# Kernel tuning notes

Hardware: AMD Instinct MI355X
Metric: run time of the kernel (lower is better)

Reference implementation:

```python
import jax, jax.numpy as jnp
import numpy as np

E, T, H, I = 64, 2048, 512, 1024


def setup_inputs() -> dict:
    key = jax.random.key(0)
    k1, k2, k3 = jax.random.split(key, 3)
    x = jax.random.normal(k1, (T, E, H), dtype=jnp.float32)
    # trunc_normal_(std=sqrt(0.1/fan_in)) approximated by normal with same std
    wi = jax.random.normal(k2, (E, H, I), dtype=jnp.float32) * (0.1 / H) ** 0.5
    wo = jax.random.normal(k3, (E, I, H), dtype=jnp.float32) * (0.1 / I) ** 0.5
    return {"x": x, "wi": wi, "wo": wo}


def reference(x, wi, wo):
    # x: [T, E, H] -> transpose to [E, T, H] (reshape(e,-1,h) is a no-op for 3D input)
    xt = jnp.transpose(x, (1, 0, 2))
    # expert GEMM 1 + exact GELU (torch nn.GELU default is erf-based)
    h = jax.nn.gelu(jnp.einsum('eth,ehi->eti', xt, wi), approximate=False)
    # dropout is skipped when expert_parallel is None; grad scalers are identity (ep_size=1)
    out = jnp.einsum('eti,eih->eth', h, wo)
    return jnp.transpose(out, (1, 0, 2))  # back to [T, E, H]
```

## Files before the change

### kernel.cpp

```cpp
#include <hip/hip_runtime.h>
#include <stdint.h>

#define NE 64
#define NT 2048
#define NH 512
#define NI 1024

typedef __attribute__((ext_vector_type(8))) short bf16x8;
typedef __attribute__((ext_vector_type(4))) float f32x4;

typedef const __attribute__((address_space(1))) void* gptr1_t;
typedef __attribute__((address_space(3))) void* lptr3_t;
#define GLOAD16(g, l) \
  __builtin_amdgcn_global_load_lds((gptr1_t)(const void*)(g), (lptr3_t)(void*)(l), 16, 0, 0)

static __device__ __forceinline__ uint16_t f2bf(float f) {
  uint32_t u = __builtin_bit_cast(uint32_t, f);
  u += 0x7fffu + ((u >> 16) & 1u);
  return (uint16_t)(u >> 16);
}

static __device__ __forceinline__ float gelu_erf(float v) {
  return 0.5f * v * (1.0f + erff(v * 0.7071067811865475f));
}

__global__ __launch_bounds__(256)
void cast_x(const float* __restrict__ x, uint16_t* __restrict__ xB,
            int t_start, int S) {
  const int total = S * NE * (NH / 8);
  for (int c = blockIdx.x * 256 + threadIdx.x; c < total; c += gridDim.x * 256) {
    const int hb = c & 63;
    const int e = (c >> 6) & 63;
    const int t = c >> 12;
    const float* ip = x + ((size_t)(t_start + t) * NE + e) * NH + (hb << 3);
    const f32x4 v0 = *(const f32x4*)ip;
    const f32x4 v1 = *(const f32x4*)(ip + 4);
    bf16x8 w;
#pragma unroll
    for (int u = 0; u < 4; ++u) {
      w[u] = (short)f2bf(v0[u]);
      w[u + 4] = (short)f2bf(v1[u]);
    }
    *(bf16x8*)&xB[((size_t)e * S + t) * NH + (hb << 3)] = w;
  }
}

__global__ __launch_bounds__(256)
void conv_tr(const float* __restrict__ in, uint16_t* __restrict__ out, int K, int N) {
  const int e = blockIdx.x;
  const int k0 = blockIdx.y << 6;
  const int n0 = blockIdx.z << 6;
  __shared__ uint16_t t[64][72];
  const int tid = threadIdx.x;
  const int r = tid >> 2;
  const int c0 = (tid & 3) << 4;
  const float* ip = in + ((size_t)e * K + k0 + r) * N + n0 + c0;
#pragma unroll
  for (int j = 0; j < 16; j += 4) {
    f32x4 v = *(const f32x4*)(ip + j);
#pragma unroll
    for (int u = 0; u < 4; ++u) t[c0 + j + u][r] = f2bf(v[u]);
  }
  __syncthreads();
  uint16_t* op = out + ((size_t)e * N + n0 + r) * K + k0 + c0;
  *(bf16x8*)op = *(const bf16x8*)&t[r][c0];
  *(bf16x8*)(op + 8) = *(const bf16x8*)&t[r][c0 + 8];
}

__global__ __launch_bounds__(256, 3)
void k_gemm1(const uint16_t* __restrict__ xB, const uint16_t* __restrict__ wiB,
             uint16_t* __restrict__ h, int Ts) {
  const int Mt = Ts >> 7;
  const int nwg = gridDim.x;
  const int wid = (blockIdx.x & 7) * (nwg >> 3) + (blockIdx.x >> 3);
  const int bn = wid & 7;
  const int bm = (wid >> 3) % Mt;
  const int be = wid / (Mt << 3);
  const int t0 = bm << 7, n0 = bn << 7;

  __shared__ __align__(16) uint16_t As[8192];
  __shared__ __align__(16) uint16_t Bs[8192];

  const int tid = threadIdx.x, lane = tid & 63;
  const int wy = (tid >> 7) & 1, wx = (tid >> 6) & 1;

  const uint16_t* Abase = xB + ((size_t)be * Ts + t0) * NH;
  const uint16_t* Bbase = wiB + ((size_t)be * NI + n0) * NH;

  int off[4], ldsOff[4];
#pragma unroll
  for (int s = 0; s < 4; ++s) {
    const int c = (s << 8) + tid;
    const int rr = c >> 3, kgs = c & 7;
    off[s] = (rr << 9) + ((kgs ^ (rr & 7)) << 3);
    ldsOff[s] = c << 4;
  }

  f32x4 acc[4][4];
#pragma unroll
  for (int i = 0; i < 4; ++i)
#pragma unroll
    for (int j = 0; j < 4; ++j) acc[i][j] = (f32x4){0.f, 0.f, 0.f, 0.f};

  const int KIT = NH >> 6;
  for (int it = 0; it < KIT; ++it) {
    __syncthreads();
#pragma unroll
    for (int s = 0; s < 4; ++s)
      GLOAD16(Abase + (it << 6) + off[s], (char*)As + ldsOff[s]);
#pragma unroll
    for (int s = 0; s < 4; ++s)
      GLOAD16(Bbase + (it << 6) + off[s], (char*)Bs + ldsOff[s]);
    __syncthreads();
#pragma unroll
    for (int ks = 0; ks < 2; ++ks) {
      const int kg = (ks << 2) + (lane >> 4);
      bf16x8 af[4], bfr[4];
#pragma unroll
      for (int mi = 0; mi < 4; ++mi) {
        const int row = (wy << 6) + (mi << 4) + (lane & 15);
        af[mi] = *(const bf16x8*)&As[(row << 6) + ((kg ^ (row & 7)) << 3)];
      }
#pragma unroll
      for (int ni = 0; ni < 4; ++ni) {
        const int col = (wx << 6) + (ni << 4) + (lane & 15);
        bfr[ni] = *(const bf16x8*)&Bs[(col << 6) + ((kg ^ (col & 7)) << 3)];
      }
#pragma unroll
      for (int mi = 0; mi < 4; ++mi)
#pragma unroll
        for (int ni = 0; ni < 4; ++ni)
          acc[mi][ni] = __builtin_amdgcn_mfma_f32_16x16x32_bf16(
              af[mi], bfr[ni], acc[mi][ni], 0, 0, 0);
    }
  }

#pragma unroll
  for (int mi = 0; mi < 4; ++mi) {
#pragma unroll
    for (int ni = 0; ni < 4; ++ni) {
      const int col = n0 + (wx << 6) + (ni << 4) + (lane & 15);
#pragma unroll
      for (int j = 0; j < 4; ++j) {
        const int r = t0 + (wy << 6) + (mi << 4) + ((lane >> 4) << 2) + j;
        h[((size_t)be * Ts + r) * NI + col] = f2bf(gelu_erf(acc[mi][ni][j]));
      }
    }
  }
}

__global__ __launch_bounds__(256, 3)
void k_gemm2(const uint16_t* __restrict__ hA, const uint16_t* __restrict__ woB,
             float* __restrict__ out, int t_start, int Ts) {
  const int Mt = Ts >> 7;
  const int nwg = gridDim.x;
  const int wid = (blockIdx.x & 7) * (nwg >> 3) + (blockIdx.x >> 3);
  const int bn = wid & 3;
  const int bm = (wid >> 2) % Mt;
  const int be = wid / (Mt << 2);
  const int t0 = bm << 7, n0 = bn << 7;

  __shared__ __align__(16) uint16_t As[8192];
  __shared__ __align__(16) uint16_t Bs[8192];

  const int tid = threadIdx.x, lane = tid & 63;
  const int wy = (tid >> 7) & 1, wx = (tid >> 6) & 1;

  const uint16_t* Abase = hA + ((size_t)be * Ts + t0) * NI;
  const uint16_t* Bbase = woB + ((size_t)be * NH + n0) * NI;

  int off[4], ldsOff[4];
#pragma unroll
  for (int s = 0; s < 4; ++s) {
    const int c = (s << 8) + tid;
    const int rr = c >> 3, kgs = c & 7;
    off[s] = (rr << 10) + ((kgs ^ (rr & 7)) << 3);
    ldsOff[s] = c << 4;
  }

  f32x4 acc[4][4];
#pragma unroll
  for (int i = 0; i < 4; ++i)
#pragma unroll
    for (int j = 0; j < 4; ++j) acc[i][j] = (f32x4){0.f, 0.f, 0.f, 0.f};

  const int KIT = NI >> 6;
  for (int it = 0; it < KIT; ++it) {
    __syncthreads();
#pragma unroll
    for (int s = 0; s < 4; ++s)
      GLOAD16(Abase + (it << 6) + off[s], (char*)As + ldsOff[s]);
#pragma unroll
    for (int s = 0; s < 4; ++s)
      GLOAD16(Bbase + (it << 6) + off[s], (char*)Bs + ldsOff[s]);
    __syncthreads();
#pragma unroll
    for (int ks = 0; ks < 2; ++ks) {
      const int kg = (ks << 2) + (lane >> 4);
      bf16x8 af[4], bfr[4];
#pragma unroll
      for (int mi = 0; mi < 4; ++mi) {
        const int row = (wy << 6) + (mi << 4) + (lane & 15);
        af[mi] = *(const bf16x8*)&As[(row << 6) + ((kg ^ (row & 7)) << 3)];
      }
#pragma unroll
      for (int ni = 0; ni < 4; ++ni) {
        const int col = (wx << 6) + (ni << 4) + (lane & 15);
        bfr[ni] = *(const bf16x8*)&Bs[(col << 6) + ((kg ^ (col & 7)) << 3)];
      }
#pragma unroll
      for (int mi = 0; mi < 4; ++mi)
#pragma unroll
        for (int ni = 0; ni < 4; ++ni)
          acc[mi][ni] = __builtin_amdgcn_mfma_f32_16x16x32_bf16(
              af[mi], bfr[ni], acc[mi][ni], 0, 0, 0);
    }
  }

#pragma unroll
  for (int mi = 0; mi < 4; ++mi) {
#pragma unroll
    for (int ni = 0; ni < 4; ++ni) {
      const int col = n0 + (wx << 6) + (ni << 4) + (lane & 15);
#pragma unroll
      for (int j = 0; j < 4; ++j) {
        const int r = t0 + (wy << 6) + (mi << 4) + ((lane >> 4) << 2) + j;
        out[((size_t)(t_start + r) * NE + be) * NH + col] = acc[mi][ni][j];
      }
    }
  }
}

extern "C" void kernel_launch(void* const* d_in, const int* in_sizes, int n_in,
                              void* d_out, int out_size, void* d_ws, size_t ws_size,
                              hipStream_t stream) {
  const float* x = (const float*)d_in[0];
  const float* wi = (const float*)d_in[1];
  const float* wo = (const float*)d_in[2];
  float* out = (float*)d_out;

  uint16_t* wiB = (uint16_t*)d_ws;
  uint16_t* woB = (uint16_t*)((char*)d_ws + 67108864);
  char* rest = (char*)d_ws + 134217728;

  const size_t perRow = (size_t)NE * NH * 2 + (size_t)NE * NI * 2;
  size_t avail = (ws_size > 134217728u) ? ws_size - 134217728u : 0;
  int Ts = (int)(avail / perRow);
  Ts &= ~127;
  if (Ts > NT) Ts = NT;
  if (Ts < 128) Ts = 128;

  uint16_t* xB = (uint16_t*)rest;
  uint16_t* h = (uint16_t*)(rest + (size_t)NE * Ts * NH * 2);

  hipLaunchKernelGGL(conv_tr, dim3(NE, NH / 64, NI / 64), dim3(256), 0, stream,
                     wi, wiB, NH, NI);
  hipLaunchKernelGGL(conv_tr, dim3(NE, NI / 64, NH / 64), dim3(256), 0, stream,
                     wo, woB, NI, NH);

  for (int ts = 0; ts < NT; ts += Ts) {
    int cur = NT - ts;
    if (cur > Ts) cur = Ts;
    const int Mt = cur >> 7;
    const int castGrid = (cur * NE * (NH / 8) + 255) / 256;
    hipLaunchKernelGGL(cast_x, dim3(castGrid < 2048 ? castGrid : 2048), dim3(256),
                       0, stream, x, xB, ts, cur);
    hipLaunchKernelGGL(k_gemm1, dim3(Mt * 8 * NE), dim3(256), 0, stream,
                       xB, wiB, h, cur);
    hipLaunchKernelGGL(k_gemm2, dim3(Mt * 4 * NE), dim3(256), 0, stream,
                       h, woB, out, ts, cur);
  }
}
```

Measured before the change: 563.9 us.

## Replace GEMM kernels with 256x256-tile double-buffered pipelined MFMA kernel

Replaces the two separate 128x128 single-buffered GEMM kernels with one templated kernel using 256x256 tiles, 512 threads (8 waves), and double-buffered LDS. Global-to-LDS loads for the next K-step are interleaved with MFMA phases using explicit waitcnt, barriers, sched_barrier, and setprio. The aim is to hide load latency and raise arithmetic intensity per workgroup. In exchange it uses 128KB of LDS and more registers, which lowers occupancy, and the tile count per expert is reduced.

Result: slower. 625.9 us (+11.0%).

```diff
diff --git a/kernel.cpp b/kernel.cpp
--- a/kernel.cpp
+++ b/kernel.cpp
@@ -67,165 +67,188 @@
   *(bf16x8*)(op + 8) = *(const bf16x8*)&t[r][c0 + 8];
 }
 
-__global__ __launch_bounds__(256, 3)
-void k_gemm1(const uint16_t* __restrict__ xB, const uint16_t* __restrict__ wiB,
-             uint16_t* __restrict__ h, int Ts) {
-  const int Mt = Ts >> 7;
+template <int KIT, int NTILES, int ASTR, int BSTR, bool GELU>
+__global__ __launch_bounds__(512, 2)
+void k_mm(const uint16_t* __restrict__ Ag, const uint16_t* __restrict__ Bg,
+          void* __restrict__ outp, int t_start, int Ts) {
+  const int Mt = Ts >> 8;
   const int nwg = gridDim.x;
-  const int wid = (blockIdx.x & 7) * (nwg >> 3) + (blockIdx.x >> 3);
-  const int bn = wid & 7;
-  const int bm = (wid >> 3) % Mt;
-  const int be = wid / (Mt << 3);
-  const int t0 = bm << 7, n0 = bn << 7;
-
-  __shared__ __align__(16) uint16_t As[8192];
-  __shared__ __align__(16) uint16_t Bs[8192];
-
-  const int tid = threadIdx.x, lane = tid & 63;
-  const int wy = (tid >> 7) & 1, wx = (tid >> 6) & 1;
-
-  const uint16_t* Abase = xB + ((size_t)be * Ts + t0) * NH;
-  const uint16_t* Bbase = wiB + ((size_t)be * NI + n0) * NH;
-
-  int off[4], ldsOff[4];
-#pragma unroll
-  for (int s = 0; s < 4; ++s) {
-    const int c = (s << 8) + tid;
-    const int rr = c >> 3, kgs = c & 7;
-    off[s] = (rr << 9) + ((kgs ^ (rr & 7)) << 3);
-    ldsOff[s] = c << 4;
-  }
-
-  f32x4 acc[4][4];
-#pragma unroll
-  for (int i = 0; i < 4; ++i)
+  const int wid_ = (blockIdx.x & 7) * (nwg >> 3) + (blockIdx.x >> 3);
+  const int bn = wid_ & (NTILES - 1);
+  const int bm = (wid_ / NTILES) % Mt;
+  const int be = wid_ / (NTILES * Mt);
+  const int t0 = bm << 8, n0 = bn << 8;
+
+  __shared__ __align__(16) uint16_t As[2][16384];
+  __shared__ __align__(16) uint16_t Bs[2][16384];
+
+  const int tid = threadIdx.x;
+  const int lane = tid & 63;
+  const int wv = tid >> 6;
+  const int wm = wv >> 2;
+  const int wn = wv & 3;
+  const int fr = lane & 15;
+  const int fq = lane >> 4;
+
+  const uint16_t* Abase = Ag + ((size_t)be * Ts + t0) * ASTR;
+  const uint16_t* Bbase = Bg + ((size_t)be * (NTILES * 256) + n0) * BSTR;
+
+  int aoff[2], boff[2];
+#pragma unroll
+  for (int s = 0; s < 2; ++s) {
+    const int c = tid + (s << 9);
+    const int row = c >> 3, g = c & 7;
+    aoff[s] = row * ASTR + ((g ^ (row & 7)) << 3);
+    boff[s] = row * BSTR + ((g ^ (row & 7)) << 3);
+  }
+
+  auto stageA = [&](int kt, int b, int h) {
+    const uint16_t* src = Abase + (size_t)(h << 7) * ASTR + (kt << 6);
+    char* dst = (char*)&As[b][0] + (h << 14) + (tid << 4);
+    GLOAD16(src + aoff[0], dst);
+    GLOAD16(src + aoff[1], dst + 8192);
+  };
+  auto stageB = [&](int kt, int b, int h) {
+    const uint16_t* src = Bbase + (size_t)(h << 7) * BSTR + (kt << 6);
+    char* dst = (char*)&Bs[b][0] + (h << 14) + (tid << 4);
+    GLOAD16(src + boff[0], dst);
+    GLOAD16(src + boff[1], dst + 8192);
+  };
+
+  auto ldsA = [&](int b, int mi, int ks) -> bf16x8 {
+    const int r = (mi << 4) + fr;
+    const int kg = ((ks << 2) + fq) ^ (fr & 7);
+    return *(const bf16x8*)&As[b][(wm << 13) + (r << 6) + (kg << 3)];
+  };
+  auto ldsB = [&](int b, int ni, int ks) -> bf16x8 {
+    const int r = ((wn & 1) << 6) + (ni << 4) + fr;
+    const int kg = ((ks << 2) + fq) ^ (fr & 7);
+    return *(const bf16x8*)&Bs[b][((wn >> 1) << 13) + (r << 6) + (kg << 3)];
+  };
+
+  f32x4 acc[8][4];
+#pragma unroll
+  for (int i = 0; i < 8; ++i)
 #pragma unroll
     for (int j = 0; j < 4; ++j) acc[i][j] = (f32x4){0.f, 0.f, 0.f, 0.f};
 
-  const int KIT = NH >> 6;
-  for (int it = 0; it < KIT; ++it) {
-    __syncthreads();
-#pragma unroll
-    for (int s = 0; s < 4; ++s)
-      GLOAD16(Abase + (it << 6) + off[s], (char*)As + ldsOff[s]);
-#pragma unroll
-    for (int s = 0; s < 4; ++s)
-      GLOAD16(Bbase + (it << 6) + off[s], (char*)Bs + ldsOff[s]);
-    __syncthreads();
-#pragma unroll
-    for (int ks = 0; ks < 2; ++ks) {
-      const int kg = (ks << 2) + (lane >> 4);
-      bf16x8 af[4], bfr[4];
-#pragma unroll
-      for (int mi = 0; mi < 4; ++mi) {
-        const int row = (wy << 6) + (mi << 4) + (lane & 15);
-        af[mi] = *(const bf16x8*)&As[(row << 6) + ((kg ^ (row & 7)) << 3)];
-      }
+  bf16x8 af[4][2], bfr[4][2];
+
+  stageA(0, 0, 0);
+  stageA(0, 0, 1);
+  stageB(0, 0, 0);
+  stageB(0, 0, 1);
+  stageB(1, 1, 0);
+  stageB(1, 1, 1);
+
+  for (int T = 0; T < KIT; ++T) {
+    const int rb = T & 1;
+    const int c1 = (T + 1 < KIT) ? T + 1 : KIT - 1;
+    const int c2 = (T + 2 < KIT) ? T + 2 : KIT - 1;
+
+    stageA(c1, (T + 1) & 1, 0);
+    asm volatile("s_waitcnt vmcnt(6)" ::: "memory");
+    __builtin_amdgcn_sched_barrier(0);
+    __builtin_amdgcn_s_barrier();
+    __builtin_amdgcn_sched_barrier(0);
+#pragma unroll
+    for (int mi = 0; mi < 4; ++mi)
+#pragma unroll
+      for (int ks = 0; ks < 2; ++ks) af[mi][ks] = ldsA(rb, mi, ks);
+#pragma unroll
+    for (int ni = 0; ni < 2; ++ni)
+#pragma unroll
+      for (int ks = 0; ks < 2; ++ks) bfr[ni][ks] = ldsB(rb, ni, ks);
+    __builtin_amdgcn_s_setprio(1);
+#pragma unroll
+    for (int mi = 0; mi < 4; ++mi)
+#pragma unroll
+      for (int ni = 0; ni < 2; ++ni)
+#pragma unroll
+        for (int ks = 0; ks < 2; ++ks)
+          acc[mi][ni] = __builtin_amdgcn_mfma_f32_16x16x32_bf16(
+              af[mi][ks], bfr[ni][ks], acc[mi][ni], 0, 0, 0);
+    __builtin_amdgcn_s_setprio(0);
+    __builtin_amdgcn_s_barrier();
+    __builtin_amdgcn_sched_barrier(0);
+
+    stageA(c1, (T + 1) & 1, 1);
+#pragma unroll
+    for (int ni = 2; ni < 4; ++ni)
+#pragma unroll
+      for (int ks = 0; ks < 2; ++ks) bfr[ni][ks] = ldsB(rb, ni, ks);
+    __builtin_amdgcn_s_setprio(1);
+#pragma unroll
+    for (int mi = 0; mi < 4; ++mi)
+#pragma unroll
+      for (int ni = 2; ni < 4; ++ni)
+#pragma unroll
+        for (int ks = 0; ks < 2; ++ks)
+          acc[mi][ni] = __builtin_amdgcn_mfma_f32_16x16x32_bf16(
+              af[mi][ks], bfr[ni][ks], acc[mi][ni], 0, 0, 0);
+    __builtin_amdgcn_s_setprio(0);
+    __builtin_amdgcn_s_barrier();
+    __builtin_amdgcn_sched_barrier(0);
+
+    stageB(c2, rb, 0);
+#pragma unroll
+    for (int mi = 0; mi < 4; ++mi)
+#pragma unroll
+      for (int ks = 0; ks < 2; ++ks) af[mi][ks] = ldsA(rb, mi + 4, ks);
+    __builtin_amdgcn_s_setprio(1);
+#pragma unroll
+    for (int mi = 0; mi < 4; ++mi)
+#pragma unroll
+      for (int ni = 0; ni < 2; ++ni)
+#pragma unroll
+        for (int ks = 0; ks < 2; ++ks)
+          acc[mi + 4][ni] = __builtin_amdgcn_mfma_f32_16x16x32_bf16(
+              af[mi][ks], bfr[ni][ks], acc[mi + 4][ni], 0, 0, 0);
+    __builtin_amdgcn_s_setprio(0);
+    __builtin_amdgcn_s_barrier();
+    __builtin_amdgcn_sched_barrier(0);
+
+    stageB(c2, rb, 1);
+    __builtin_amdgcn_s_setprio(1);
+#pragma unroll
+    for (int mi = 0; mi < 4; ++mi)
+#pragma unroll
+      for (int ni = 2; ni < 4; ++ni)
+#pragma unroll
+        for (int ks = 0; ks < 2; ++ks)
+          acc[mi + 4][ni] = __builtin_amdgcn_mfma_f32_16x16x32_bf16(
+              af[mi][ks], bfr[ni][ks], acc[mi + 4][ni], 0, 0, 0);
+    __builtin_amdgcn_s_setprio(0);
+    __builtin_amdgcn_s_barrier();
+    __builtin_amdgcn_sched_barrier(0);
+  }
+
+  if constexpr (GELU) {
+    uint16_t* hp = (uint16_t*)outp;
+#pragma unroll
+    for (int mi = 0; mi < 8; ++mi) {
 #pragma unroll
       for (int ni = 0; ni < 4; ++ni) {
-        const int col = (wx << 6) + (ni << 4) + (lane & 15);
-        bfr[ni] = *(const bf16x8*)&Bs[(col << 6) + ((kg ^ (col & 7)) << 3)];
-      }
-#pragma unroll
-      for (int mi = 0; mi < 4; ++mi)
-#pragma unroll
-        for (int ni = 0; ni < 4; ++ni)
-          acc[mi][ni] = __builtin_amdgcn_mfma_f32_16x16x32_bf16(
-              af[mi], bfr[ni], acc[mi][ni], 0, 0, 0);
-    }
-  }
-
-#pragma unroll
-  for (int mi = 0; mi < 4; ++mi) {
-#pragma unroll
-    for (int ni = 0; ni < 4; ++ni) {
-      const int col = n0 + (wx << 6) + (ni << 4) + (lane & 15);
-#pragma unroll
-      for (int j = 0; j < 4; ++j) {
-        const int r = t0 + (wy << 6) + (mi << 4) + ((lane >> 4) << 2) + j;
-        h[((size_t)be * Ts + r) * NI + col] = f2bf(gelu_erf(acc[mi][ni][j]));
+        const int col = n0 + (wn << 6) + (ni << 4) + fr;
+#pragma unroll
+        for (int j = 0; j < 4; ++j) {
+          const int row = t0 + (wm << 7) + (mi << 4) + (fq << 2) + j;
+          hp[((size_t)be * Ts + row) * NI + col] = f2bf(gelu_erf(acc[mi][ni][j]));
+        }
       }
     }
-  }
-}
-
-__global__ __launch_bounds__(256, 3)
-void k_gemm2(const uint16_t* __restrict__ hA, const uint16_t* __restrict__ woB,
-             float* __restrict__ out, int t_start, int Ts) {
-  const int Mt = Ts >> 7;
-  const int nwg = gridDim.x;
-  const int wid = (blockIdx.x & 7) * (nwg >> 3) + (blockIdx.x >> 3);
-  const int bn = wid & 3;
-  const int bm = (wid >> 2) % Mt;
-  const int be = wid / (Mt << 2);
-  const int t0 = bm << 7, n0 = bn << 7;
-
-  __shared__ __align__(16) uint16_t As[8192];
-  __shared__ __align__(16) uint16_t Bs[8192];
-
-  const int tid = threadIdx.x, lane = tid & 63;
-  const int wy = (tid >> 7) & 1, wx = (tid >> 6) & 1;
-
-  const uint16_t* Abase = hA + ((size_t)be * Ts + t0) * NI;
-  const uint16_t* Bbase = woB + ((size_t)be * NH + n0) * NI;
-
-  int off[4], ldsOff[4];
-#pragma unroll
-  for (int s = 0; s < 4; ++s) {
-    const int c = (s << 8) + tid;
-    const int rr = c >> 3, kgs = c & 7;
-    off[s] = (rr << 10) + ((kgs ^ (rr & 7)) << 3);
-    ldsOff[s] = c << 4;
-  }
-
-  f32x4 acc[4][4];
-#pragma unroll
-  for (int i = 0; i < 4; ++i)
-#pragma unroll
-    for (int j = 0; j < 4; ++j) acc[i][j] = (f32x4){0.f, 0.f, 0.f, 0.f};
-
-  const int KIT = NI >> 6;
-  for (int it = 0; it < KIT; ++it) {
-    __syncthreads();
-#pragma unroll
-    for (int s = 0; s < 4; ++s)
-      GLOAD16(Abase + (it << 6) + off[s], (char*)As + ldsOff[s]);
-#pragma unroll
-    for (int s = 0; s < 4; ++s)
-      GLOAD16(Bbase + (it << 6) + off[s], (char*)Bs + ldsOff[s]);
-    __syncthreads();
-#pragma unroll
-    for (int ks = 0; ks < 2; ++ks) {
-      const int kg = (ks << 2) + (lane >> 4);
-      bf16x8 af[4], bfr[4];
-#pragma unroll
-      for (int mi = 0; mi < 4; ++mi) {
-        const int row = (wy << 6) + (mi << 4) + (lane & 15);
-        af[mi] = *(const bf16x8*)&As[(row << 6) + ((kg ^ (row & 7)) << 3)];
-      }
+  } else {
+    float* op = (float*)outp;
+#pragma unroll
+    for (int mi = 0; mi < 8; ++mi) {
 #pragma unroll
       for (int ni = 0; ni < 4; ++ni) {
-        const int col = (wx << 6) + (ni << 4) + (lane & 15);
-        bfr[ni] = *(const bf16x8*)&Bs[(col << 6) + ((kg ^ (col & 7)) << 3)];
-      }
-#pragma unroll
-      for (int mi = 0; mi < 4; ++mi)
-#pragma unroll
-        for (int ni = 0; ni < 4; ++ni)
-          acc[mi][ni] = __builtin_amdgcn_mfma_f32_16x16x32_bf16(
-              af[mi], bfr[ni], acc[mi][ni], 0, 0, 0);
-    }
-  }
-
-#pragma unroll
-  for (int mi = 0; mi < 4; ++mi) {
-#pragma unroll
-    for (int ni = 0; ni < 4; ++ni) {
-      const int col = n0 + (wx << 6) + (ni << 4) + (lane & 15);
-#pragma unroll
-      for (int j = 0; j < 4; ++j) {
-        const int r = t0 + (wy << 6) + (mi << 4) + ((lane >> 4) << 2) + j;
-        out[((size_t)(t_start + r) * NE + be) * NH + col] = acc[mi][ni][j];
+        const int col = n0 + (wn << 6) + (ni << 4) + fr;
+#pragma unroll
+        for (int j = 0; j < 4; ++j) {
+          const int row = t0 + (wm << 7) + (mi << 4) + (fq << 2) + j;
+          op[((size_t)(t_start + row) * NE + be) * NH + col] = acc[mi][ni][j];
+        }
       }
     }
   }
@@ -246,12 +269,9 @@
   const size_t perRow = (size_t)NE * NH * 2 + (size_t)NE * NI * 2;
   size_t avail = (ws_size > 134217728u) ? ws_size - 134217728u : 0;
   int Ts = (int)(avail / perRow);
-  Ts &= ~127;
+  Ts &= ~255;
   if (Ts > NT) Ts = NT;
-  if (Ts < 128) Ts = 128;
-
-  uint16_t* xB = (uint16_t*)rest;
-  uint16_t* h = (uint16_t*)(rest + (size_t)NE * Ts * NH * 2);
+  if (Ts < 256) Ts = 256;
 
   hipLaunchKernelGGL(conv_tr, dim3(NE, NH / 64, NI / 64), dim3(256), 0, stream,
                      wi, wiB, NH, NI);
@@ -261,13 +281,15 @@
   for (int ts = 0; ts < NT; ts += Ts) {
     int cur = NT - ts;
     if (cur > Ts) cur = Ts;
-    const int Mt = cur >> 7;
+    const int Mt = cur >> 8;
+    uint16_t* xB = (uint16_t*)rest;
+    uint16_t* h = (uint16_t*)(rest + (size_t)NE * cur * NH * 2);
     const int castGrid = (cur * NE * (NH / 8) + 255) / 256;
     hipLaunchKernelGGL(cast_x, dim3(castGrid < 2048 ? castGrid : 2048), dim3(256),
                        0, stream, x, xB, ts, cur);
-    hipLaunchKernelGGL(k_gemm1, dim3(Mt * 8 * NE), dim3(256), 0, stream,
-                       xB, wiB, h, cur);
-    hipLaunchKernelGGL(k_gemm2, dim3(Mt * 4 * NE), dim3(256), 0, stream,
-                       h, woB, out, ts, cur);
-  }
-}
+    hipLaunchKernelGGL((k_mm<8, 4, NH, NH, true>), dim3(Mt * 4 * NE), dim3(512),
+                       0, stream, xB, wiB, (void*)h, 0, cur);
+    hipLaunchKernelGGL((k_mm<16, 2, NI, NI, false>), dim3(Mt * 2 * NE), dim3(512),
+                       0, stream, h, woB, (void*)out, ts, cur);
+  }
+}
```

## Load B fragments directly from global into registers with double-buffered prefetch

Applied to the files above, without the earlier changes.

Merges the two GEMM kernels into one template and stops staging the weight (B) tile through LDS. Each wave now reads its B fragments straight from global memory into registers, double-buffered so the next k-step's B loads overlap the current MFMA work. Only A still goes through LDS, which halves LDS use and LDS traffic. The cost is uncoalesced-ish 16-byte global reads of B with no reuse between the two wy waves, plus higher register pressure from two B buffers at a 3-waves occupancy target.

Result: slower. 793.1 us (+40.6%).

```diff
diff --git a/kernel.cpp b/kernel.cpp
--- a/kernel.cpp
+++ b/kernel.cpp
@@ -67,165 +67,114 @@
   *(bf16x8*)(op + 8) = *(const bf16x8*)&t[r][c0 + 8];
 }
 
+template <int KIT, int NTILES, int STR, bool GELU>
 __global__ __launch_bounds__(256, 3)
-void k_gemm1(const uint16_t* __restrict__ xB, const uint16_t* __restrict__ wiB,
-             uint16_t* __restrict__ h, int Ts) {
+void k_mm(const uint16_t* __restrict__ Ag, const uint16_t* __restrict__ Bg,
+          void* __restrict__ outp, int t_start, int Ts) {
   const int Mt = Ts >> 7;
   const int nwg = gridDim.x;
   const int wid = (blockIdx.x & 7) * (nwg >> 3) + (blockIdx.x >> 3);
-  const int bn = wid & 7;
-  const int bm = (wid >> 3) % Mt;
-  const int be = wid / (Mt << 3);
+  const int bn = wid & (NTILES - 1);
+  const int bm = (wid / NTILES) % Mt;
+  const int be = wid / (NTILES * Mt);
   const int t0 = bm << 7, n0 = bn << 7;
 
   __shared__ __align__(16) uint16_t As[8192];
-  __shared__ __align__(16) uint16_t Bs[8192];
 
   const int tid = threadIdx.x, lane = tid & 63;
   const int wy = (tid >> 7) & 1, wx = (tid >> 6) & 1;
-
-  const uint16_t* Abase = xB + ((size_t)be * Ts + t0) * NH;
-  const uint16_t* Bbase = wiB + ((size_t)be * NI + n0) * NH;
-
-  int off[4], ldsOff[4];
+  const int fr = lane & 15, fq = lane >> 4;
+
+  const uint16_t* Abase = Ag + ((size_t)be * Ts + t0) * STR;
+  const uint16_t* Bbase = Bg + ((size_t)be * (NTILES * 128) + n0) * STR;
+
+  int aoff[4], ldsOff[4];
 #pragma unroll
   for (int s = 0; s < 4; ++s) {
     const int c = (s << 8) + tid;
     const int rr = c >> 3, kgs = c & 7;
-    off[s] = (rr << 9) + ((kgs ^ (rr & 7)) << 3);
+    aoff[s] = rr * STR + ((kgs ^ (rr & 7)) << 3);
     ldsOff[s] = c << 4;
   }
 
+  const uint16_t* bp[4];
+#pragma unroll
+  for (int ni = 0; ni < 4; ++ni)
+    bp[ni] = Bbase + (size_t)((wx << 6) + (ni << 4) + fr) * STR + (fq << 3);
+
   f32x4 acc[4][4];
 #pragma unroll
   for (int i = 0; i < 4; ++i)
 #pragma unroll
     for (int j = 0; j < 4; ++j) acc[i][j] = (f32x4){0.f, 0.f, 0.f, 0.f};
 
-  const int KIT = NH >> 6;
-  for (int it = 0; it < KIT; ++it) {
-    __syncthreads();
+  bf16x8 b0[4][2], b1[4][2];
+
+  auto stageA = [&](int it) {
 #pragma unroll
     for (int s = 0; s < 4; ++s)
-      GLOAD16(Abase + (it << 6) + off[s], (char*)As + ldsOff[s]);
-#pragma unroll
-    for (int s = 0; s < 4; ++s)
-      GLOAD16(Bbase + (it << 6) + off[s], (char*)Bs + ldsOff[s]);
-    __syncthreads();
-#pragma unroll
-    for (int ks = 0; ks < 2; ++ks) {
-      const int kg = (ks << 2) + (lane >> 4);
-      bf16x8 af[4], bfr[4];
-#pragma unroll
-      for (int mi = 0; mi < 4; ++mi) {
-        const int row = (wy << 6) + (mi << 4) + (lane & 15);
-        af[mi] = *(const bf16x8*)&As[(row << 6) + ((kg ^ (row & 7)) << 3)];
-      }
+      GLOAD16(Abase + (it << 6) + aoff[s], (char*)As + ldsOff[s]);
+  };
+#define LOADB(buf, it)                                                        \
+  _Pragma("unroll") for (int ni = 0; ni < 4; ++ni)                            \
+      _Pragma("unroll") for (int ks = 0; ks < 2; ++ks)                        \
+          buf[ni][ks] = *(const bf16x8*)(bp[ni] + ((it) << 6) + (ks << 5));
+#define COMPUTE(buf)                                                          \
+  _Pragma("unroll") for (int ks = 0; ks < 2; ++ks) {                          \
+    const int kg = (ks << 2) + fq;                                            \
+    bf16x8 af[4];                                                             \
+    _Pragma("unroll") for (int mi = 0; mi < 4; ++mi) {                        \
+      const int row = (wy << 6) + (mi << 4) + fr;                             \
+      af[mi] = *(const bf16x8*)&As[(row << 6) + ((kg ^ (row & 7)) << 3)];     \
+    }                                                                         \
+    _Pragma("unroll") for (int mi = 0; mi < 4; ++mi)                          \
+        _Pragma("unroll") for (int ni = 0; ni < 4; ++ni)                      \
+            acc[mi][ni] = __builtin_amdgcn_mfma_f32_16x16x32_bf16(            \
+                af[mi], buf[ni][ks], acc[mi][ni], 0, 0, 0);                   \
+  }
+
+  LOADB(b0, 0);
+  for (int it = 0; it < KIT; it += 2) {
+    __syncthreads();
+    stageA(it);
+    __syncthreads();
+    LOADB(b1, it + 1);
+    COMPUTE(b0);
+    __syncthreads();
+    stageA(it + 1);
+    __syncthreads();
+    if (it + 2 < KIT) LOADB(b0, it + 2);
+    COMPUTE(b1);
+  }
+#undef LOADB
+#undef COMPUTE
+
+  if constexpr (GELU) {
+    uint16_t* hp = (uint16_t*)outp;
+#pragma unroll
+    for (int mi = 0; mi < 4; ++mi) {
 #pragma unroll
       for (int ni = 0; ni < 4; ++ni) {
-        const int col = (wx << 6) + (ni << 4) + (lane & 15);
-        bfr[ni] = *(const bf16x8*)&Bs[(col << 6) + ((kg ^ (col & 7)) << 3)];
-      }
-#pragma unroll
-      for (int mi = 0; mi < 4; ++mi)
-#pragma unroll
-        for (int ni = 0; ni < 4; ++ni)
-          acc[mi][ni] = __builtin_amdgcn_mfma_f32_16x16x32_bf16(
-              af[mi], bfr[ni], acc[mi][ni], 0, 0, 0);
-    }
-  }
-
-#pragma unroll
-  for (int mi = 0; mi < 4; ++mi) {
-#pragma unroll
-    for (int ni = 0; ni < 4; ++ni) {
-      const int col = n0 + (wx << 6) + (ni << 4) + (lane & 15);
-#pragma unroll
-      for (int j = 0; j < 4; ++j) {
-        const int r = t0 + (wy << 6) + (mi << 4) + ((lane >> 4) << 2) + j;
-        h[((size_t)be * Ts + r) * NI + col] = f2bf(gelu_erf(acc[mi][ni][j]));
+        const int col = n0 + (wx << 6) + (ni << 4) + fr;
+#pragma unroll
+        for (int j = 0; j < 4; ++j) {
+          const int r = t0 + (wy << 6) + (mi << 4) + (fq << 2) + j;
+          hp[((size_t)be * Ts + r) * NI + col] = f2bf(gelu_erf(acc[mi][ni][j]));
+        }
       }
     }
-  }
-}
-
-__global__ __launch_bounds__(256, 3)
-void k_gemm2(const uint16_t* __restrict__ hA, const uint16_t* __restrict__ woB,
-             float* __restrict__ out, int t_start, int Ts) {
-  const int Mt = Ts >> 7;
-  const int nwg = gridDim.x;
-  const int wid = (blockIdx.x & 7) * (nwg >> 3) + (blockIdx.x >> 3);
-  const int bn = wid & 3;
-  const int bm = (wid >> 2) % Mt;
-  const int be = wid / (Mt << 2);
-  const int t0 = bm << 7, n0 = bn << 7;
-
-  __shared__ __align__(16) uint16_t As[8192];
-  __shared__ __align__(16) uint16_t Bs[8192];
-
-  const int tid = threadIdx.x, lane = tid & 63;
-  const int wy = (tid >> 7) & 1, wx = (tid >> 6) & 1;
-
-  const uint16_t* Abase = hA + ((size_t)be * Ts + t0) * NI;
-  const uint16_t* Bbase = woB + ((size_t)be * NH + n0) * NI;
-
-  int off[4], ldsOff[4];
-#pragma unroll
-  for (int s = 0; s < 4; ++s) {
-    const int c = (s << 8) + tid;
-    const int rr = c >> 3, kgs = c & 7;
-    off[s] = (rr << 10) + ((kgs ^ (rr & 7)) << 3);
-    ldsOff[s] = c << 4;
-  }
-
-  f32x4 acc[4][4];
-#pragma unroll
-  for (int i = 0; i < 4; ++i)
-#pragma unroll
-    for (int j = 0; j < 4; ++j) acc[i][j] = (f32x4){0.f, 0.f, 0.f, 0.f};
-
-  const int KIT = NI >> 6;
-  for (int it = 0; it < KIT; ++it) {
-    __syncthreads();
-#pragma unroll
-    for (int s = 0; s < 4; ++s)
-      GLOAD16(Abase + (it << 6) + off[s], (char*)As + ldsOff[s]);
-#pragma unroll
-    for (int s = 0; s < 4; ++s)
-      GLOAD16(Bbase + (it << 6) + off[s], (char*)Bs + ldsOff[s]);
-    __syncthreads();
-#pragma unroll
-    for (int ks = 0; ks < 2; ++ks) {
-      const int kg = (ks << 2) + (lane >> 4);
-      bf16x8 af[4], bfr[4];
-#pragma unroll
-      for (int mi = 0; mi < 4; ++mi) {
-        const int row = (wy << 6) + (mi << 4) + (lane & 15);
-        af[mi] = *(const bf16x8*)&As[(row << 6) + ((kg ^ (row & 7)) << 3)];
-      }
+  } else {
+    float* op = (float*)outp;
+#pragma unroll
+    for (int mi = 0; mi < 4; ++mi) {
 #pragma unroll
       for (int ni = 0; ni < 4; ++ni) {
-        const int col = (wx << 6) + (ni << 4) + (lane & 15);
-        bfr[ni] = *(const bf16x8*)&Bs[(col << 6) + ((kg ^ (col & 7)) << 3)];
-      }
-#pragma unroll
-      for (int mi = 0; mi < 4; ++mi)
-#pragma unroll
-        for (int ni = 0; ni < 4; ++ni)
-          acc[mi][ni] = __builtin_amdgcn_mfma_f32_16x16x32_bf16(
-              af[mi], bfr[ni], acc[mi][ni], 0, 0, 0);
-    }
-  }
-
-#pragma unroll
-  for (int mi = 0; mi < 4; ++mi) {
-#pragma unroll
-    for (int ni = 0; ni < 4; ++ni) {
-      const int col = n0 + (wx << 6) + (ni << 4) + (lane & 15);
-#pragma unroll
-      for (int j = 0; j < 4; ++j) {
-        const int r = t0 + (wy << 6) + (mi << 4) + ((lane >> 4) << 2) + j;
-        out[((size_t)(t_start + r) * NE + be) * NH + col] = acc[mi][ni][j];
+        const int col = n0 + (wx << 6) + (ni << 4) + fr;
+#pragma unroll
+        for (int j = 0; j < 4; ++j) {
+          const int r = t0 + (wy << 6) + (mi << 4) + (fq << 2) + j;
+          op[((size_t)(t_start + r) * NE + be) * NH + col] = acc[mi][ni][j];
+        }
       }
     }
   }
@@ -250,9 +199,6 @@
   if (Ts > NT) Ts = NT;
   if (Ts < 128) Ts = 128;
 
-  uint16_t* xB = (uint16_t*)rest;
-  uint16_t* h = (uint16_t*)(rest + (size_t)NE * Ts * NH * 2);
-
   hipLaunchKernelGGL(conv_tr, dim3(NE, NH / 64, NI / 64), dim3(256), 0, stream,
                      wi, wiB, NH, NI);
   hipLaunchKernelGGL(conv_tr, dim3(NE, NI / 64, NH / 64), dim3(256), 0, stream,
@@ -262,12 +208,14 @@
     int cur = NT - ts;
     if (cur > Ts) cur = Ts;
     const int Mt = cur >> 7;
+    uint16_t* xB = (uint16_t*)rest;
+    uint16_t* h = (uint16_t*)(rest + (size_t)NE * cur * NH * 2);
     const int castGrid = (cur * NE * (NH / 8) + 255) / 256;
     hipLaunchKernelGGL(cast_x, dim3(castGrid < 2048 ? castGrid : 2048), dim3(256),
                        0, stream, x, xB, ts, cur);
-    hipLaunchKernelGGL(k_gemm1, dim3(Mt * 8 * NE), dim3(256), 0, stream,
-                       xB, wiB, h, cur);
-    hipLaunchKernelGGL(k_gemm2, dim3(Mt * 4 * NE), dim3(256), 0, stream,
-                       h, woB, out, ts, cur);
-  }
-}
+    hipLaunchKernelGGL((k_mm<8, 8, NH, true>), dim3(Mt * 8 * NE), dim3(256),
+                       0, stream, xB, wiB, (void*)h, 0, cur);
+    hipLaunchKernelGGL((k_mm<16, 4, NI, false>), dim3(Mt * 4 * NE), dim3(256),
+                       0, stream, h, woB, (void*)out, ts, cur);
+  }
+}
```

## Cast x once up front, cap token chunks at 512, use tanh-form GELU

Applied to the files above, without the earlier changes.

All of x is now cast to bf16 in a single launch before the chunk loop instead of once per chunk, and the GEMM1 A pointer indexes into the full buffer by t_start. Token chunks for the h intermediate are capped at 512 so the h buffer stays small and may stay cache-resident between GEMM1 and GEMM2. The exact erf GELU is replaced with a tanh-based approximation built on __expf, which cuts epilogue cost but departs slightly from the exact erf reference. The cap also means more chunk iterations and launches.

Result: slower. 678.5 us (+20.3%).

```diff
diff --git a/kernel.cpp b/kernel.cpp
--- a/kernel.cpp
+++ b/kernel.cpp
@@ -20,19 +20,21 @@
   return (uint16_t)(u >> 16);
 }
 
-static __device__ __forceinline__ float gelu_erf(float v) {
-  return 0.5f * v * (1.0f + erff(v * 0.7071067811865475f));
+static __device__ __forceinline__ float gelu_fast(float x) {
+  const float x3 = x * x * x;
+  const float twoy = 1.5957691216057308f * x + 0.07135481627f * x3;
+  const float e = __expf(twoy);
+  return x - x / (e + 1.0f);
 }
 
 __global__ __launch_bounds__(256)
-void cast_x(const float* __restrict__ x, uint16_t* __restrict__ xB,
-            int t_start, int S) {
-  const int total = S * NE * (NH / 8);
+void cast_x(const float* __restrict__ x, uint16_t* __restrict__ xB) {
+  const int total = NT * NE * (NH / 8);
   for (int c = blockIdx.x * 256 + threadIdx.x; c < total; c += gridDim.x * 256) {
     const int hb = c & 63;
     const int e = (c >> 6) & 63;
     const int t = c >> 12;
-    const float* ip = x + ((size_t)(t_start + t) * NE + e) * NH + (hb << 3);
+    const float* ip = x + ((size_t)t * NE + e) * NH + (hb << 3);
     const f32x4 v0 = *(const f32x4*)ip;
     const f32x4 v1 = *(const f32x4*)(ip + 4);
     bf16x8 w;
@@ -41,7 +43,7 @@
       w[u] = (short)f2bf(v0[u]);
       w[u + 4] = (short)f2bf(v1[u]);
     }
-    *(bf16x8*)&xB[((size_t)e * S + t) * NH + (hb << 3)] = w;
+    *(bf16x8*)&xB[((size_t)e * NT + t) * NH + (hb << 3)] = w;
   }
 }
 
@@ -69,8 +71,8 @@
 
 __global__ __launch_bounds__(256, 3)
 void k_gemm1(const uint16_t* __restrict__ xB, const uint16_t* __restrict__ wiB,
-             uint16_t* __restrict__ h, int Ts) {
-  const int Mt = Ts >> 7;
+             uint16_t* __restrict__ h, int t_start, int TsS) {
+  const int Mt = TsS >> 7;
   const int nwg = gridDim.x;
   const int wid = (blockIdx.x & 7) * (nwg >> 3) + (blockIdx.x >> 3);
   const int bn = wid & 7;
@@ -84,7 +86,7 @@
   const int tid = threadIdx.x, lane = tid & 63;
   const int wy = (tid >> 7) & 1, wx = (tid >> 6) & 1;
 
-  const uint16_t* Abase = xB + ((size_t)be * Ts + t0) * NH;
+  const uint16_t* Abase = xB + ((size_t)be * NT + t_start + t0) * NH;
   const uint16_t* Bbase = wiB + ((size_t)be * NI + n0) * NH;
 
   int off[4], ldsOff[4];
@@ -143,7 +145,7 @@
 #pragma unroll
       for (int j = 0; j < 4; ++j) {
         const int r = t0 + (wy << 6) + (mi << 4) + ((lane >> 4) << 2) + j;
-        h[((size_t)be * Ts + r) * NI + col] = f2bf(gelu_erf(acc[mi][ni][j]));
+        h[((size_t)be * TsS + r) * NI + col] = f2bf(gelu_fast(acc[mi][ni][j]));
       }
     }
   }
@@ -151,8 +153,8 @@
 
 __global__ __launch_bounds__(256, 3)
 void k_gemm2(const uint16_t* __restrict__ hA, const uint16_t* __restrict__ woB,
-             float* __restrict__ out, int t_start, int Ts) {
-  const int Mt = Ts >> 7;
+             float* __restrict__ out, int t_start, int TsS) {
+  const int Mt = TsS >> 7;
   const int nwg = gridDim.x;
   const int wid = (blockIdx.x & 7) * (nwg >> 3) + (blockIdx.x >> 3);
   const int bn = wid & 3;
@@ -166,7 +168,7 @@
   const int tid = threadIdx.x, lane = tid & 63;
   const int wy = (tid >> 7) & 1, wx = (tid >> 6) & 1;
 
-  const uint16_t* Abase = hA + ((size_t)be * Ts + t0) * NI;
+  const uint16_t* Abase = hA + ((size_t)be * TsS + t0) * NI;
   const uint16_t* Bbase = woB + ((size_t)be * NH + n0) * NI;
 
   int off[4], ldsOff[4];
@@ -241,32 +243,28 @@
 
   uint16_t* wiB = (uint16_t*)d_ws;
   uint16_t* woB = (uint16_t*)((char*)d_ws + 67108864);
-  char* rest = (char*)d_ws + 134217728;
-
-  const size_t perRow = (size_t)NE * NH * 2 + (size_t)NE * NI * 2;
-  size_t avail = (ws_size > 134217728u) ? ws_size - 134217728u : 0;
-  int Ts = (int)(avail / perRow);
+  uint16_t* xB = (uint16_t*)((char*)d_ws + 134217728);
+  uint16_t* h = (uint16_t*)((char*)d_ws + 134217728 + (size_t)NE * NT * NH * 2);
+
+  const size_t fixed = 134217728u + (size_t)NE * NT * NH * 2;
+  size_t avail = (ws_size > fixed) ? ws_size - fixed : 0;
+  int Ts = (int)(avail / ((size_t)NE * NI * 2));
+  if (Ts > 512) Ts = 512;
   Ts &= ~127;
-  if (Ts > NT) Ts = NT;
   if (Ts < 128) Ts = 128;
-
-  uint16_t* xB = (uint16_t*)rest;
-  uint16_t* h = (uint16_t*)(rest + (size_t)NE * Ts * NH * 2);
 
   hipLaunchKernelGGL(conv_tr, dim3(NE, NH / 64, NI / 64), dim3(256), 0, stream,
                      wi, wiB, NH, NI);
   hipLaunchKernelGGL(conv_tr, dim3(NE, NI / 64, NH / 64), dim3(256), 0, stream,
                      wo, woB, NI, NH);
+  hipLaunchKernelGGL(cast_x, dim3(2048), dim3(256), 0, stream, x, xB);
 
   for (int ts = 0; ts < NT; ts += Ts) {
     int cur = NT - ts;
     if (cur > Ts) cur = Ts;
     const int Mt = cur >> 7;
-    const int castGrid = (cur * NE * (NH / 8) + 255) / 256;
-    hipLaunchKernelGGL(cast_x, dim3(castGrid < 2048 ? castGrid : 2048), dim3(256),
-                       0, stream, x, xB, ts, cur);
     hipLaunchKernelGGL(k_gemm1, dim3(Mt * 8 * NE), dim3(256), 0, stream,
-                       xB, wiB, h, cur);
+                       xB, wiB, h, ts, cur);
     hipLaunchKernelGGL(k_gemm2, dim3(Mt * 4 * NE), dim3(256), 0, stream,
                        h, woB, out, ts, cur);
   }
```
